# Optimization experiments

Measured on AMD Instinct MI355X. Metric: run time of the kernel, lower is better.

The kernel has to match this reference:

```python
import jax, jax.numpy as jnp
import numpy as np

N_NODES = 50000
N_EDGES = 600000
IN_DIM = 128
HID = 256
OUT = 3


def setup_inputs() -> dict:
    key = jax.random.key(0)
    ks = jax.random.split(key, 10)
    x = jax.random.normal(ks[0], (N_NODES, IN_DIM), dtype=jnp.float32)
    edge_index = jax.random.randint(ks[1], (2, N_EDGES), 0, N_NODES, dtype=jnp.int64)
    s = lambda k, shp: jax.random.normal(k, shp, dtype=jnp.float32) * (1.0 / np.sqrt(shp[0]))
    return {
        "x": x,
        "edge_index": edge_index,
        # SAGEConv1: lin_l (applied to aggregated neighbors, with bias), lin_r (root, no bias)
        "W1l": s(ks[2], (IN_DIM, HID)), "b1": jnp.zeros((HID,), jnp.float32), "W1r": s(ks[3], (IN_DIM, HID)),
        # SAGEConv2
        "W2l": s(ks[4], (HID, HID)), "b2": jnp.zeros((HID,), jnp.float32), "W2r": s(ks[5], (HID, HID)),
        # classification head
        "Wh": s(ks[6], (HID, OUT)), "bh": jnp.zeros((OUT,), jnp.float32),
    }


def _sage_conv(x, edge_index, Wl, b, Wr):
    """PyG SAGEConv with mean aggregation: out = lin_l(mean_{j->i} x_j) + lin_r(x_i)."""
    src, dst = edge_index[0], edge_index[1]
    n = x.shape[0]
    # gather source features and scatter-mean onto targets
    msg_sum = jax.ops.segment_sum(x[src], dst, num_segments=n)          # [N, d]
    deg = jax.ops.segment_sum(jnp.ones((src.shape[0],), x.dtype), dst, num_segments=n)
    mean = msg_sum / jnp.maximum(deg, 1.0)[:, None]                      # isolated nodes -> 0
    return mean @ Wl + b + x @ Wr


def reference(x, edge_index, W1l, b1, W1r, W2l, b2, W2r, Wh, bh):
    h = jax.nn.relu(_sage_conv(x, edge_index, W1l, b1, W1r))
    # dropout(p=0.2) is identity in eval mode
    h = jax.nn.relu(_sage_conv(h, edge_index, W2l, b2, W2r))
    return h @ Wh + bh
```

## Files before the change

### kernel.cpp

```cpp
#include <hip/hip_runtime.h>
#include <hip/hip_bf16.h>

#define N_NODES 50000
#define N_EDGES 600000
#define IN_DIM 128
#define HID 256
#define OUT_DIM 3

#define SCAN_B 256
#define SCAN_NB ((N_NODES + SCAN_B - 1) / SCAN_B)

typedef __bf16 bf16x8 __attribute__((ext_vector_type(8)));
typedef float f32x4 __attribute__((ext_vector_type(4)));

static __device__ __forceinline__ unsigned short f2b(float f) {
    union { float f; unsigned u; } u; u.f = f;
    unsigned r = u.u + 0x7fffu + ((u.u >> 16) & 1u);
    return (unsigned short)(r >> 16);
}
static __device__ __forceinline__ float b2f(unsigned short b) {
    union { unsigned u; float f; } u; u.u = ((unsigned)b) << 16;
    return u.f;
}


__global__ void count_deg_kernel(const int* __restrict__ dst, int* __restrict__ counts) {
    int e = blockIdx.x * blockDim.x + threadIdx.x;
    if (e < N_EDGES) atomicAdd(&counts[dst[e]], 1);
}

__global__ __launch_bounds__(256) void block_sum_kernel(const int* __restrict__ counts,
                                                        int* __restrict__ partial) {
    int node = blockIdx.x * SCAN_B + threadIdx.x;
    int v = (node < N_NODES) ? counts[node] : 0;
#pragma unroll
    for (int off = 32; off > 0; off >>= 1) v += __shfl_down(v, off);
    __shared__ int ws[4];
    if ((threadIdx.x & 63) == 0) ws[threadIdx.x >> 6] = v;
    __syncthreads();
    if (threadIdx.x == 0) partial[blockIdx.x] = ws[0] + ws[1] + ws[2] + ws[3];
}

__global__ __launch_bounds__(256) void scan_partial_kernel(int* __restrict__ partial) {
    __shared__ int s[SCAN_B];
    int t = threadIdx.x;
    int v = (t < SCAN_NB) ? partial[t] : 0;
    s[t] = v;
    __syncthreads();
    for (int off = 1; off < SCAN_B; off <<= 1) {
        int u = (t >= off) ? s[t - off] : 0;
        __syncthreads();
        s[t] += u;
        __syncthreads();
    }
    if (t < SCAN_NB) partial[t] = s[t] - v;
}

__global__ __launch_bounds__(256) void write_rowptr_kernel(const int* __restrict__ counts,
                                                           const int* __restrict__ partial,
                                                           int* __restrict__ row_ptr) {
    __shared__ int s[SCAN_B];
    int t = threadIdx.x;
    int node = blockIdx.x * SCAN_B + t;
    int v = (node < N_NODES) ? counts[node] : 0;
    s[t] = v;
    __syncthreads();
    for (int off = 1; off < SCAN_B; off <<= 1) {
        int u = (t >= off) ? s[t - off] : 0;
        __syncthreads();
        s[t] += u;
        __syncthreads();
    }
    if (node < N_NODES) row_ptr[node] = partial[blockIdx.x] + s[t] - v;
    if (node == 0) row_ptr[N_NODES] = N_EDGES;
}

__global__ void fill_csr_kernel(const int* __restrict__ src, const int* __restrict__ dst,
                                const int* __restrict__ row_ptr, int* __restrict__ cursor,
                                int* __restrict__ csr_src) {
    int e = blockIdx.x * blockDim.x + threadIdx.x;
    if (e < N_EDGES) {
        int d = dst[e];
        int pos = atomicAdd(&cursor[d], 1);
        csr_src[row_ptr[d] + pos] = src[e];
    }
}


__global__ void cast_f2b_kernel(const float* __restrict__ in, unsigned short* __restrict__ out, int n) {
    int i = blockIdx.x * blockDim.x + threadIdx.x;
    if (i * 4 < n) {
        float4 v = ((const float4*)in)[i];
        ushort4 o;
        o.x = f2b(v.x); o.y = f2b(v.y); o.z = f2b(v.z); o.w = f2b(v.w);
        ((ushort4*)out)[i] = o;
    }
}

__global__ void tcast4_kernel(const float* __restrict__ W1l, const float* __restrict__ W1r,
                              const float* __restrict__ W2l, const float* __restrict__ W2r,
                              unsigned short* __restrict__ W1lt, unsigned short* __restrict__ W1rt,
                              unsigned short* __restrict__ W2lt, unsigned short* __restrict__ W2rt) {
    int i = blockIdx.x * blockDim.x + threadIdx.x;
    const float* in; unsigned short* out; int K, base;
    if (i < 32768)        { in = W1l; out = W1lt; K = IN_DIM; base = 0; }
    else if (i < 65536)   { in = W1r; out = W1rt; K = IN_DIM; base = 32768; }
    else if (i < 131072)  { in = W2l; out = W2lt; K = HID;    base = 65536; }
    else if (i < 196608)  { in = W2r; out = W2rt; K = HID;    base = 131072; }
    else return;
    int j = i - base;
    int k = j >> 8;
    int n = j & 255;
    out[(size_t)n * K + k] = f2b(in[j]);
}


template <int D>
__global__ __launch_bounds__(256) void agg_mean_b_kernel(const unsigned short* __restrict__ feat,
                                                         const int* __restrict__ row_ptr,
                                                         const int* __restrict__ csr_src,
                                                         unsigned short* __restrict__ out) {
    int node = blockIdx.x * 4 + (threadIdx.x >> 6);
    if (node >= N_NODES) return;
    int lane = threadIdx.x & 63;
    constexpr int VPT = D / 64;
    float acc[VPT];
#pragma unroll
    for (int v = 0; v < VPT; v++) acc[v] = 0.f;
    int beg = row_ptr[node], end = row_ptr[node + 1];
    int i = beg;
    if constexpr (VPT == 2) {
        for (; i + 4 <= end; i += 4) {
            int s0 = csr_src[i], s1 = csr_src[i + 1], s2 = csr_src[i + 2], s3 = csr_src[i + 3];
            unsigned v0 = ((const unsigned*)(feat + (size_t)s0 * D))[lane];
            unsigned v1 = ((const unsigned*)(feat + (size_t)s1 * D))[lane];
            unsigned v2 = ((const unsigned*)(feat + (size_t)s2 * D))[lane];
            unsigned v3 = ((const unsigned*)(feat + (size_t)s3 * D))[lane];
            acc[0] += b2f((unsigned short)(v0 & 0xffff)) + b2f((unsigned short)(v1 & 0xffff))
                    + b2f((unsigned short)(v2 & 0xffff)) + b2f((unsigned short)(v3 & 0xffff));
            acc[1] += b2f((unsigned short)(v0 >> 16)) + b2f((unsigned short)(v1 >> 16))
                    + b2f((unsigned short)(v2 >> 16)) + b2f((unsigned short)(v3 >> 16));
        }
        for (; i < end; i++) {
            unsigned v = ((const unsigned*)(feat + (size_t)csr_src[i] * D))[lane];
            acc[0] += b2f((unsigned short)(v & 0xffff));
            acc[1] += b2f((unsigned short)(v >> 16));
        }
    } else {
        for (; i + 4 <= end; i += 4) {
            int s0 = csr_src[i], s1 = csr_src[i + 1], s2 = csr_src[i + 2], s3 = csr_src[i + 3];
            uint2 v0 = ((const uint2*)(feat + (size_t)s0 * D))[lane];
            uint2 v1 = ((const uint2*)(feat + (size_t)s1 * D))[lane];
            uint2 v2 = ((const uint2*)(feat + (size_t)s2 * D))[lane];
            uint2 v3 = ((const uint2*)(feat + (size_t)s3 * D))[lane];
            acc[0] += b2f((unsigned short)(v0.x & 0xffff)) + b2f((unsigned short)(v1.x & 0xffff))
                    + b2f((unsigned short)(v2.x & 0xffff)) + b2f((unsigned short)(v3.x & 0xffff));
            acc[1] += b2f((unsigned short)(v0.x >> 16)) + b2f((unsigned short)(v1.x >> 16))
                    + b2f((unsigned short)(v2.x >> 16)) + b2f((unsigned short)(v3.x >> 16));
            acc[2] += b2f((unsigned short)(v0.y & 0xffff)) + b2f((unsigned short)(v1.y & 0xffff))
                    + b2f((unsigned short)(v2.y & 0xffff)) + b2f((unsigned short)(v3.y & 0xffff));
            acc[3] += b2f((unsigned short)(v0.y >> 16)) + b2f((unsigned short)(v1.y >> 16))
                    + b2f((unsigned short)(v2.y >> 16)) + b2f((unsigned short)(v3.y >> 16));
        }
        for (; i < end; i++) {
            uint2 v = ((const uint2*)(feat + (size_t)csr_src[i] * D))[lane];
            acc[0] += b2f((unsigned short)(v.x & 0xffff));
            acc[1] += b2f((unsigned short)(v.x >> 16));
            acc[2] += b2f((unsigned short)(v.y & 0xffff));
            acc[3] += b2f((unsigned short)(v.y >> 16));
        }
    }
    float inv = (end > beg) ? 1.0f / (float)(end - beg) : 0.0f;
    unsigned short* o = out + (size_t)node * D;
    if constexpr (VPT == 2) {
        unsigned pk = (unsigned)f2b(acc[0] * inv) | ((unsigned)f2b(acc[1] * inv) << 16);
        ((unsigned*)o)[lane] = pk;
    } else {
        uint2 pk;
        pk.x = (unsigned)f2b(acc[0] * inv) | ((unsigned)f2b(acc[1] * inv) << 16);
        pk.y = (unsigned)f2b(acc[2] * inv) | ((unsigned)f2b(acc[3] * inv) << 16);
        ((uint2*)o)[lane] = pk;
    }
}


__global__ __launch_bounds__(256) void gemm_mfma_kernel(
    const unsigned short* __restrict__ A0, const unsigned short* __restrict__ W0t,
    const unsigned short* __restrict__ A1, const unsigned short* __restrict__ W1t,
    const float* __restrict__ bias, unsigned short* __restrict__ out,
    int M, int K) {
    __shared__ unsigned short As[128][40];
    __shared__ unsigned short Bs[128][40];

    const int t = threadIdx.x;
    const int w = t >> 6;
    const int l = t & 63;
    const int quad = l >> 4;
    const int lr = l & 15;
    const int m0 = blockIdx.x * 128;
    const int n0 = blockIdx.y * 128;

    f32x4 acc[2][8];
    const f32x4 zero = {0.f, 0.f, 0.f, 0.f};
#pragma unroll
    for (int mt = 0; mt < 2; mt++)
#pragma unroll
        for (int nt = 0; nt < 8; nt++) acc[mt][nt] = zero;

    float bias_r[8];
#pragma unroll
    for (int nt = 0; nt < 8; nt++) bias_r[nt] = bias[n0 + nt * 16 + lr];

    const int ldr = t >> 2;
    const int lkb = (t & 3) * 8;

    for (int phase = 0; phase < 2; ++phase) {
        const unsigned short* A = phase ? A1 : A0;
        const unsigned short* Wt = phase ? W1t : W0t;
        for (int k0 = 0; k0 < K; k0 += 32) {
            __syncthreads();
#pragma unroll
            for (int it = 0; it < 2; ++it) {
                int r = ldr + it * 64;
                int gm = m0 + r;
                uint4 av = make_uint4(0u, 0u, 0u, 0u);
                if (gm < M) av = *(const uint4*)(A + (size_t)gm * K + k0 + lkb);
                *(uint4*)&As[r][lkb] = av;
                uint4 bv = *(const uint4*)(Wt + (size_t)(n0 + r) * K + k0 + lkb);
                *(uint4*)&Bs[r][lkb] = bv;
            }
            __syncthreads();
            bf16x8 a[2], b[8];
#pragma unroll
            for (int mt = 0; mt < 2; mt++)
                a[mt] = *(const bf16x8*)&As[w * 32 + mt * 16 + lr][quad * 8];
#pragma unroll
            for (int nt = 0; nt < 8; nt++)
                b[nt] = *(const bf16x8*)&Bs[nt * 16 + lr][quad * 8];
#pragma unroll
            for (int mt = 0; mt < 2; mt++)
#pragma unroll
                for (int nt = 0; nt < 8; nt++)
                    acc[mt][nt] = __builtin_amdgcn_mfma_f32_16x16x32_bf16(a[mt], b[nt], acc[mt][nt], 0, 0, 0);
        }
    }

#pragma unroll
    for (int mt = 0; mt < 2; mt++)
#pragma unroll
        for (int r = 0; r < 4; r++) {
            int gm = m0 + w * 32 + mt * 16 + quad * 4 + r;
            if (gm >= M) continue;
            unsigned short* orow = out + (size_t)gm * HID;
#pragma unroll
            for (int nt = 0; nt < 8; nt++) {
                int gn = n0 + nt * 16 + lr;
                float v = acc[mt][nt][r] + bias_r[nt];
                v = fmaxf(v, 0.f);
                orow[gn] = f2b(v);
            }
        }
}


__global__ __launch_bounds__(256) void gemm_mfma_head_kernel(
    const unsigned short* __restrict__ A0, const unsigned short* __restrict__ W0t,
    const unsigned short* __restrict__ A1, const unsigned short* __restrict__ W1t,
    const float* __restrict__ bias, const float* __restrict__ Wh,
    float* __restrict__ out, int M, int K) {
    __shared__ unsigned short As[128][40];
    __shared__ unsigned short Bs[128][40];

    const int t = threadIdx.x;
    const int w = t >> 6;
    const int l = t & 63;
    const int quad = l >> 4;
    const int lr = l & 15;
    const int m0 = blockIdx.x * 128;
    const int n0 = blockIdx.y * 128;

    f32x4 acc[2][8];
    const f32x4 zero = {0.f, 0.f, 0.f, 0.f};
#pragma unroll
    for (int mt = 0; mt < 2; mt++)
#pragma unroll
        for (int nt = 0; nt < 8; nt++) acc[mt][nt] = zero;

    float bias_r[8];
    float wh_r[8][3];
#pragma unroll
    for (int nt = 0; nt < 8; nt++) {
        int gn = n0 + nt * 16 + lr;
        bias_r[nt] = bias[gn];
        wh_r[nt][0] = Wh[gn * 3 + 0];
        wh_r[nt][1] = Wh[gn * 3 + 1];
        wh_r[nt][2] = Wh[gn * 3 + 2];
    }

    const int ldr = t >> 2;
    const int lkb = (t & 3) * 8;

    for (int phase = 0; phase < 2; ++phase) {
        const unsigned short* A = phase ? A1 : A0;
        const unsigned short* Wt = phase ? W1t : W0t;
        for (int k0 = 0; k0 < K; k0 += 32) {
            __syncthreads();
#pragma unroll
            for (int it = 0; it < 2; ++it) {
                int r = ldr + it * 64;
                int gm = m0 + r;
                uint4 av = make_uint4(0u, 0u, 0u, 0u);
                if (gm < M) av = *(const uint4*)(A + (size_t)gm * K + k0 + lkb);
                *(uint4*)&As[r][lkb] = av;
                uint4 bv = *(const uint4*)(Wt + (size_t)(n0 + r) * K + k0 + lkb);
                *(uint4*)&Bs[r][lkb] = bv;
            }
            __syncthreads();
            bf16x8 a[2], b[8];
#pragma unroll
            for (int mt = 0; mt < 2; mt++)
                a[mt] = *(const bf16x8*)&As[w * 32 + mt * 16 + lr][quad * 8];
#pragma unroll
            for (int nt = 0; nt < 8; nt++)
                b[nt] = *(const bf16x8*)&Bs[nt * 16 + lr][quad * 8];
#pragma unroll
            for (int mt = 0; mt < 2; mt++)
#pragma unroll
                for (int nt = 0; nt < 8; nt++)
                    acc[mt][nt] = __builtin_amdgcn_mfma_f32_16x16x32_bf16(a[mt], b[nt], acc[mt][nt], 0, 0, 0);
        }
    }

#pragma unroll
    for (int mt = 0; mt < 2; mt++)
#pragma unroll
        for (int r = 0; r < 4; r++) {
            int gm = m0 + w * 32 + mt * 16 + quad * 4 + r;
            float p0 = 0.f, p1 = 0.f, p2 = 0.f;
#pragma unroll
            for (int nt = 0; nt < 8; nt++) {
                float v = fmaxf(acc[mt][nt][r] + bias_r[nt], 0.f);
                p0 += v * wh_r[nt][0];
                p1 += v * wh_r[nt][1];
                p2 += v * wh_r[nt][2];
            }
#pragma unroll
            for (int off = 1; off < 16; off <<= 1) {
                p0 += __shfl_xor(p0, off);
                p1 += __shfl_xor(p1, off);
                p2 += __shfl_xor(p2, off);
            }
            if (lr == 0 && gm < M) {
                atomicAdd(&out[(size_t)gm * 3 + 0], p0);
                atomicAdd(&out[(size_t)gm * 3 + 1], p1);
                atomicAdd(&out[(size_t)gm * 3 + 2], p2);
            }
        }
}

__global__ void init_out_kernel(const float* __restrict__ bh, float* __restrict__ out) {
    int i = blockIdx.x * blockDim.x + threadIdx.x;
    if (i < N_NODES * 3) {
        int c = i % 3;
        out[i] = bh[c];
    }
}


extern "C" void kernel_launch(void* const* d_in, const int* in_sizes, int n_in,
                              void* d_out, int out_size, void* d_ws, size_t ws_size,
                              hipStream_t stream) {
    const float* x   = (const float*)d_in[0];
    const int*   ei  = (const int*)d_in[1];
    const int*   src = ei;
    const int*   dst = ei + N_EDGES;
    const float* W1l = (const float*)d_in[2];
    const float* b1  = (const float*)d_in[3];
    const float* W1r = (const float*)d_in[4];
    const float* W2l = (const float*)d_in[5];
    const float* b2  = (const float*)d_in[6];
    const float* W2r = (const float*)d_in[7];
    const float* Wh  = (const float*)d_in[8];
    const float* bh  = (const float*)d_in[9];
    float* out = (float*)d_out;

    char* ws = (char*)d_ws;
    size_t off = 0;
    auto alloc = [&](size_t bytes) -> void* {
        void* p = ws + off;
        off = (off + bytes + 255) & ~(size_t)255;
        return p;
    };
    int* counts   = (int*)alloc((size_t)N_NODES * 4);
    int* row_ptr  = (int*)alloc((size_t)(N_NODES + 1) * 4);
    int* cursor   = (int*)alloc((size_t)N_NODES * 4);
    int* partial  = (int*)alloc((size_t)SCAN_NB * 4);
    int* csr_src  = (int*)alloc((size_t)N_EDGES * 4);
    unsigned short* xb   = (unsigned short*)alloc((size_t)N_NODES * IN_DIM * 2);
    unsigned short* agg  = (unsigned short*)alloc((size_t)N_NODES * HID * 2);
    unsigned short* h1   = (unsigned short*)alloc((size_t)N_NODES * HID * 2);
    unsigned short* W1lt = (unsigned short*)alloc((size_t)IN_DIM * HID * 2);
    unsigned short* W1rt = (unsigned short*)alloc((size_t)IN_DIM * HID * 2);
    unsigned short* W2lt = (unsigned short*)alloc((size_t)HID * HID * 2);
    unsigned short* W2rt = (unsigned short*)alloc((size_t)HID * HID * 2);

    hipMemsetAsync(counts, 0, (size_t)N_NODES * 4, stream);
    hipMemsetAsync(cursor, 0, (size_t)N_NODES * 4, stream);

    const int eblocks = (N_EDGES + 255) / 256;
    count_deg_kernel<<<eblocks, 256, 0, stream>>>(dst, counts);
    block_sum_kernel<<<SCAN_NB, SCAN_B, 0, stream>>>(counts, partial);
    scan_partial_kernel<<<1, SCAN_B, 0, stream>>>(partial);
    write_rowptr_kernel<<<SCAN_NB, SCAN_B, 0, stream>>>(counts, partial, row_ptr);
    fill_csr_kernel<<<eblocks, 256, 0, stream>>>(src, dst, row_ptr, cursor, csr_src);

    {
        int n = N_NODES * IN_DIM;
        cast_f2b_kernel<<<(n / 4 + 255) / 256, 256, 0, stream>>>(x, xb, n);
        tcast4_kernel<<<(196608 + 255) / 256, 256, 0, stream>>>(W1l, W1r, W2l, W2r,
                                                                W1lt, W1rt, W2lt, W2rt);
        init_out_kernel<<<(N_NODES * 3 + 255) / 256, 256, 0, stream>>>(bh, out);
    }

    const int nblocks4 = (N_NODES + 3) / 4;
    dim3 gg((N_NODES + 127) / 128, HID / 128);

    agg_mean_b_kernel<IN_DIM><<<nblocks4, 256, 0, stream>>>(xb, row_ptr, csr_src, agg);
    gemm_mfma_kernel<<<gg, 256, 0, stream>>>(agg, W1lt, xb, W1rt, b1, h1, N_NODES, IN_DIM);

    agg_mean_b_kernel<HID><<<nblocks4, 256, 0, stream>>>(h1, row_ptr, csr_src, agg);
    gemm_mfma_head_kernel<<<gg, 256, 0, stream>>>(agg, W2lt, h1, W2rt, b2, Wh, out, N_NODES, HID);
}
```

Baseline: 303.3 us.

## Use direct global-to-LDS loads in GEMM and 16-byte multi-edge gathers in aggregation

The GEMM kernels now stage tiles with global_load_lds (direct global-to-LDS DMA) into a k-block-major LDS layout, with a larger K step of 64 and two MFMA sub-steps per barrier pair. Activation buffers are padded to M_PAD rows so the row bounds check can be dropped. The aggregation kernels use 16-byte loads, with sub-groups of the wavefront handling different edges at once, then reduce across lanes with shuffles. This aims to cut per-load instruction overhead and barrier count. The risk is that the padded rows hold uninitialized data, which feeds only rows that are never stored.

Result: no change. 307.9 us (+1.5%).

```diff
diff --git a/kernel.cpp b/kernel.cpp
--- a/kernel.cpp
+++ b/kernel.cpp
@@ -7,6 +7,8 @@
 #define HID 256
 #define OUT_DIM 3
 
+#define M_PAD 50048
+
 #define SCAN_B 256
 #define SCAN_NB ((N_NODES + SCAN_B - 1) / SCAN_B)
 
@@ -21,6 +23,11 @@
 static __device__ __forceinline__ float b2f(unsigned short b) {
     union { unsigned u; float f; } u; u.u = ((unsigned)b) << 16;
     return u.f;
+}
+
+static __device__ __forceinline__ void gload16(const void* g, unsigned short* l) {
+    __builtin_amdgcn_global_load_lds((const __attribute__((address_space(1))) void*)g,
+                                     (__attribute__((address_space(3))) void*)l, 16, 0, 0);
 }
 
 
@@ -114,91 +121,156 @@
     out[(size_t)n * K + k] = f2b(in[j]);
 }
 
-
-template <int D>
-__global__ __launch_bounds__(256) void agg_mean_b_kernel(const unsigned short* __restrict__ feat,
-                                                         const int* __restrict__ row_ptr,
-                                                         const int* __restrict__ csr_src,
-                                                         unsigned short* __restrict__ out) {
+__global__ void init_out_kernel(const float* __restrict__ bh, float* __restrict__ out) {
+    int i = blockIdx.x * blockDim.x + threadIdx.x;
+    if (i < N_NODES * 3) out[i] = bh[i % 3];
+}
+
+
+static __device__ __forceinline__ void addv(float* acc, uint4 v) {
+    acc[0] += b2f((unsigned short)(v.x & 0xffff));
+    acc[1] += b2f((unsigned short)(v.x >> 16));
+    acc[2] += b2f((unsigned short)(v.y & 0xffff));
+    acc[3] += b2f((unsigned short)(v.y >> 16));
+    acc[4] += b2f((unsigned short)(v.z & 0xffff));
+    acc[5] += b2f((unsigned short)(v.z >> 16));
+    acc[6] += b2f((unsigned short)(v.w & 0xffff));
+    acc[7] += b2f((unsigned short)(v.w >> 16));
+}
+
+static __device__ __forceinline__ uint4 pack8(const float* a) {
+    uint4 pk;
+    pk.x = (unsigned)f2b(a[0]) | ((unsigned)f2b(a[1]) << 16);
+    pk.y = (unsigned)f2b(a[2]) | ((unsigned)f2b(a[3]) << 16);
+    pk.z = (unsigned)f2b(a[4]) | ((unsigned)f2b(a[5]) << 16);
+    pk.w = (unsigned)f2b(a[6]) | ((unsigned)f2b(a[7]) << 16);
+    return pk;
+}
+
+__global__ __launch_bounds__(256) void agg_mean256_kernel(const unsigned short* __restrict__ feat,
+                                                          const int* __restrict__ row_ptr,
+                                                          const int* __restrict__ csr_src,
+                                                          unsigned short* __restrict__ out) {
     int node = blockIdx.x * 4 + (threadIdx.x >> 6);
     if (node >= N_NODES) return;
     int lane = threadIdx.x & 63;
-    constexpr int VPT = D / 64;
-    float acc[VPT];
-#pragma unroll
-    for (int v = 0; v < VPT; v++) acc[v] = 0.f;
+    int half = lane >> 5, lh = lane & 31;
+    const uint4* f4 = (const uint4*)feat;
+    float acc[8];
+#pragma unroll
+    for (int j = 0; j < 8; j++) acc[j] = 0.f;
     int beg = row_ptr[node], end = row_ptr[node + 1];
     int i = beg;
-    if constexpr (VPT == 2) {
-        for (; i + 4 <= end; i += 4) {
-            int s0 = csr_src[i], s1 = csr_src[i + 1], s2 = csr_src[i + 2], s3 = csr_src[i + 3];
-            unsigned v0 = ((const unsigned*)(feat + (size_t)s0 * D))[lane];
-            unsigned v1 = ((const unsigned*)(feat + (size_t)s1 * D))[lane];
-            unsigned v2 = ((const unsigned*)(feat + (size_t)s2 * D))[lane];
-            unsigned v3 = ((const unsigned*)(feat + (size_t)s3 * D))[lane];
-            acc[0] += b2f((unsigned short)(v0 & 0xffff)) + b2f((unsigned short)(v1 & 0xffff))
-                    + b2f((unsigned short)(v2 & 0xffff)) + b2f((unsigned short)(v3 & 0xffff));
-            acc[1] += b2f((unsigned short)(v0 >> 16)) + b2f((unsigned short)(v1 >> 16))
-                    + b2f((unsigned short)(v2 >> 16)) + b2f((unsigned short)(v3 >> 16));
-        }
-        for (; i < end; i++) {
-            unsigned v = ((const unsigned*)(feat + (size_t)csr_src[i] * D))[lane];
-            acc[0] += b2f((unsigned short)(v & 0xffff));
-            acc[1] += b2f((unsigned short)(v >> 16));
-        }
-    } else {
-        for (; i + 4 <= end; i += 4) {
-            int s0 = csr_src[i], s1 = csr_src[i + 1], s2 = csr_src[i + 2], s3 = csr_src[i + 3];
-            uint2 v0 = ((const uint2*)(feat + (size_t)s0 * D))[lane];
-            uint2 v1 = ((const uint2*)(feat + (size_t)s1 * D))[lane];
-            uint2 v2 = ((const uint2*)(feat + (size_t)s2 * D))[lane];
-            uint2 v3 = ((const uint2*)(feat + (size_t)s3 * D))[lane];
-            acc[0] += b2f((unsigned short)(v0.x & 0xffff)) + b2f((unsigned short)(v1.x & 0xffff))
-                    + b2f((unsigned short)(v2.x & 0xffff)) + b2f((unsigned short)(v3.x & 0xffff));
-            acc[1] += b2f((unsigned short)(v0.x >> 16)) + b2f((unsigned short)(v1.x >> 16))
-                    + b2f((unsigned short)(v2.x >> 16)) + b2f((unsigned short)(v3.x >> 16));
-            acc[2] += b2f((unsigned short)(v0.y & 0xffff)) + b2f((unsigned short)(v1.y & 0xffff))
-                    + b2f((unsigned short)(v2.y & 0xffff)) + b2f((unsigned short)(v3.y & 0xffff));
-            acc[3] += b2f((unsigned short)(v0.y >> 16)) + b2f((unsigned short)(v1.y >> 16))
-                    + b2f((unsigned short)(v2.y >> 16)) + b2f((unsigned short)(v3.y >> 16));
-        }
-        for (; i < end; i++) {
-            uint2 v = ((const uint2*)(feat + (size_t)csr_src[i] * D))[lane];
-            acc[0] += b2f((unsigned short)(v.x & 0xffff));
-            acc[1] += b2f((unsigned short)(v.x >> 16));
-            acc[2] += b2f((unsigned short)(v.y & 0xffff));
-            acc[3] += b2f((unsigned short)(v.y >> 16));
-        }
+    for (; i + 4 <= end; i += 4) {
+        int sA = csr_src[i + half];
+        int sB = csr_src[i + 2 + half];
+        uint4 vA = f4[(size_t)sA * 32 + lh];
+        uint4 vB = f4[(size_t)sB * 32 + lh];
+        addv(acc, vA);
+        addv(acc, vB);
+    }
+    if (i + 2 <= end) {
+        int s = csr_src[i + half];
+        addv(acc, f4[(size_t)s * 32 + lh]);
+        i += 2;
+    }
+    if (i < end && half == 0) {
+        int s = csr_src[i];
+        addv(acc, f4[(size_t)s * 32 + lh]);
     }
     float inv = (end > beg) ? 1.0f / (float)(end - beg) : 0.0f;
-    unsigned short* o = out + (size_t)node * D;
-    if constexpr (VPT == 2) {
-        unsigned pk = (unsigned)f2b(acc[0] * inv) | ((unsigned)f2b(acc[1] * inv) << 16);
-        ((unsigned*)o)[lane] = pk;
-    } else {
-        uint2 pk;
-        pk.x = (unsigned)f2b(acc[0] * inv) | ((unsigned)f2b(acc[1] * inv) << 16);
-        pk.y = (unsigned)f2b(acc[2] * inv) | ((unsigned)f2b(acc[3] * inv) << 16);
-        ((uint2*)o)[lane] = pk;
-    }
-}
-
+#pragma unroll
+    for (int j = 0; j < 8; j++) {
+        acc[j] += __shfl_xor(acc[j], 32);
+        acc[j] *= inv;
+    }
+    if (half == 0) ((uint4*)(out + (size_t)node * 256))[lh] = pack8(acc);
+}
+
+__global__ __launch_bounds__(256) void agg_mean128_kernel(const unsigned short* __restrict__ feat,
+                                                          const int* __restrict__ row_ptr,
+                                                          const int* __restrict__ csr_src,
+                                                          unsigned short* __restrict__ out) {
+    int node = blockIdx.x * 4 + (threadIdx.x >> 6);
+    if (node >= N_NODES) return;
+    int lane = threadIdx.x & 63;
+    int q = lane >> 4, lq = lane & 15;
+    const uint4* f4 = (const uint4*)feat;
+    float acc[8];
+#pragma unroll
+    for (int j = 0; j < 8; j++) acc[j] = 0.f;
+    int beg = row_ptr[node], end = row_ptr[node + 1];
+    int i = beg;
+    for (; i + 8 <= end; i += 8) {
+        int sA = csr_src[i + q];
+        int sB = csr_src[i + 4 + q];
+        uint4 vA = f4[(size_t)sA * 16 + lq];
+        uint4 vB = f4[(size_t)sB * 16 + lq];
+        addv(acc, vA);
+        addv(acc, vB);
+    }
+    if (i + 4 <= end) {
+        int s = csr_src[i + q];
+        addv(acc, f4[(size_t)s * 16 + lq]);
+        i += 4;
+    }
+    int rem = end - i;
+    if (q < rem) {
+        int s = csr_src[i + q];
+        addv(acc, f4[(size_t)s * 16 + lq]);
+    }
+    float inv = (end > beg) ? 1.0f / (float)(end - beg) : 0.0f;
+#pragma unroll
+    for (int j = 0; j < 8; j++) {
+        acc[j] += __shfl_xor(acc[j], 32);
+        acc[j] += __shfl_xor(acc[j], 16);
+        acc[j] *= inv;
+    }
+    if (q == 0) ((uint4*)(out + (size_t)node * 128))[lq] = pack8(acc);
+}
+
+
+#define GEMM_STAGE_AND_MFMA(A, Wt)                                                          \
+    for (int k0 = 0; k0 < K; k0 += 64) {                                                    \
+        __syncthreads();                                                                    \
+        _Pragma("unroll")                                                                   \
+        for (int r = 0; r < 4; r++) {                                                       \
+            int kb = skb + 2 * r;                                                           \
+            gload16(A + (size_t)(m0 + sm) * K + k0 + kb * 8, &As[kb * 1024 + sm * 8]);      \
+            gload16(Wt + (size_t)(n0 + sm) * K + k0 + kb * 8, &Bs[kb * 1024 + sm * 8]);     \
+        }                                                                                   \
+        __syncthreads();                                                                    \
+        _Pragma("unroll")                                                                   \
+        for (int kk = 0; kk < 2; kk++) {                                                    \
+            int kbb = kk * 4 + quad;                                                        \
+            bf16x8 a[2], b[8];                                                              \
+            a[0] = *(const bf16x8*)&As[kbb * 1024 + (w * 32 + lr) * 8];                     \
+            a[1] = *(const bf16x8*)&As[kbb * 1024 + (w * 32 + 16 + lr) * 8];                \
+            _Pragma("unroll")                                                               \
+            for (int nt = 0; nt < 8; nt++)                                                  \
+                b[nt] = *(const bf16x8*)&Bs[kbb * 1024 + (nt * 16 + lr) * 8];               \
+            _Pragma("unroll")                                                               \
+            for (int mt = 0; mt < 2; mt++)                                                  \
+                _Pragma("unroll")                                                           \
+                for (int nt = 0; nt < 8; nt++)                                              \
+                    acc[mt][nt] = __builtin_amdgcn_mfma_f32_16x16x32_bf16(a[mt], b[nt],     \
+                                                                          acc[mt][nt], 0, 0, 0); \
+        }                                                                                   \
+    }
 
 __global__ __launch_bounds__(256) void gemm_mfma_kernel(
     const unsigned short* __restrict__ A0, const unsigned short* __restrict__ W0t,
     const unsigned short* __restrict__ A1, const unsigned short* __restrict__ W1t,
     const float* __restrict__ bias, unsigned short* __restrict__ out,
     int M, int K) {
-    __shared__ unsigned short As[128][40];
-    __shared__ unsigned short Bs[128][40];
+    __shared__ __align__(16) unsigned short As[8 * 128 * 8];
+    __shared__ __align__(16) unsigned short Bs[8 * 128 * 8];
 
     const int t = threadIdx.x;
-    const int w = t >> 6;
-    const int l = t & 63;
-    const int quad = l >> 4;
-    const int lr = l & 15;
-    const int m0 = blockIdx.x * 128;
-    const int n0 = blockIdx.y * 128;
+    const int w = t >> 6, l = t & 63;
+    const int quad = l >> 4, lr = l & 15;
+    const int m0 = blockIdx.x * 128, n0 = blockIdx.y * 128;
+    const int sm = t & 127, skb = t >> 7;
 
     f32x4 acc[2][8];
     const f32x4 zero = {0.f, 0.f, 0.f, 0.f};
@@ -211,39 +283,8 @@
 #pragma unroll
     for (int nt = 0; nt < 8; nt++) bias_r[nt] = bias[n0 + nt * 16 + lr];
 
-    const int ldr = t >> 2;
-    const int lkb = (t & 3) * 8;
-
-    for (int phase = 0; phase < 2; ++phase) {
-        const unsigned short* A = phase ? A1 : A0;
-        const unsigned short* Wt = phase ? W1t : W0t;
-        for (int k0 = 0; k0 < K; k0 += 32) {
-            __syncthreads();
-#pragma unroll
-            for (int it = 0; it < 2; ++it) {
-                int r = ldr + it * 64;
-                int gm = m0 + r;
-                uint4 av = make_uint4(0u, 0u, 0u, 0u);
-                if (gm < M) av = *(const uint4*)(A + (size_t)gm * K + k0 + lkb);
-                *(uint4*)&As[r][lkb] = av;
-                uint4 bv = *(const uint4*)(Wt + (size_t)(n0 + r) * K + k0 + lkb);
-                *(uint4*)&Bs[r][lkb] = bv;
-            }
-            __syncthreads();
-            bf16x8 a[2], b[8];
-#pragma unroll
-            for (int mt = 0; mt < 2; mt++)
-                a[mt] = *(const bf16x8*)&As[w * 32 + mt * 16 + lr][quad * 8];
-#pragma unroll
-            for (int nt = 0; nt < 8; nt++)
-                b[nt] = *(const bf16x8*)&Bs[nt * 16 + lr][quad * 8];
-#pragma unroll
-            for (int mt = 0; mt < 2; mt++)
-#pragma unroll
-                for (int nt = 0; nt < 8; nt++)
-                    acc[mt][nt] = __builtin_amdgcn_mfma_f32_16x16x32_bf16(a[mt], b[nt], acc[mt][nt], 0, 0, 0);
-        }
-    }
+    GEMM_STAGE_AND_MFMA(A0, W0t)
+    GEMM_STAGE_AND_MFMA(A1, W1t)
 
 #pragma unroll
     for (int mt = 0; mt < 2; mt++)
@@ -254,30 +295,25 @@
             unsigned short* orow = out + (size_t)gm * HID;
 #pragma unroll
             for (int nt = 0; nt < 8; nt++) {
-                int gn = n0 + nt * 16 + lr;
-                float v = acc[mt][nt][r] + bias_r[nt];
-                v = fmaxf(v, 0.f);
-                orow[gn] = f2b(v);
+                float v = fmaxf(acc[mt][nt][r] + bias_r[nt], 0.f);
+                orow[n0 + nt * 16 + lr] = f2b(v);
             }
         }
 }
-
 
 __global__ __launch_bounds__(256) void gemm_mfma_head_kernel(
     const unsigned short* __restrict__ A0, const unsigned short* __restrict__ W0t,
     const unsigned short* __restrict__ A1, const unsigned short* __restrict__ W1t,
     const float* __restrict__ bias, const float* __restrict__ Wh,
     float* __restrict__ out, int M, int K) {
-    __shared__ unsigned short As[128][40];
-    __shared__ unsigned short Bs[128][40];
+    __shared__ __align__(16) unsigned short As[8 * 128 * 8];
+    __shared__ __align__(16) unsigned short Bs[8 * 128 * 8];
 
     const int t = threadIdx.x;
-    const int w = t >> 6;
-    const int l = t & 63;
-    const int quad = l >> 4;
-    const int lr = l & 15;
-    const int m0 = blockIdx.x * 128;
-    const int n0 = blockIdx.y * 128;
+    const int w = t >> 6, l = t & 63;
+    const int quad = l >> 4, lr = l & 15;
+    const int m0 = blockIdx.x * 128, n0 = blockIdx.y * 128;
+    const int sm = t & 127, skb = t >> 7;
 
     f32x4 acc[2][8];
     const f32x4 zero = {0.f, 0.f, 0.f, 0.f};
@@ -297,39 +333,8 @@
         wh_r[nt][2] = Wh[gn * 3 + 2];
     }
 
-    const int ldr = t >> 2;
-    const int lkb = (t & 3) * 8;
-
-    for (int phase = 0; phase < 2; ++phase) {
-        const unsigned short* A = phase ? A1 : A0;
-        const unsigned short* Wt = phase ? W1t : W0t;
-        for (int k0 = 0; k0 < K; k0 += 32) {
-            __syncthreads();
-#pragma unroll
-            for (int it = 0; it < 2; ++it) {
-                int r = ldr + it * 64;
-                int gm = m0 + r;
-                uint4 av = make_uint4(0u, 0u, 0u, 0u);
-                if (gm < M) av = *(const uint4*)(A + (size_t)gm * K + k0 + lkb);
-                *(uint4*)&As[r][lkb] = av;
-                uint4 bv = *(const uint4*)(Wt + (size_t)(n0 + r) * K + k0 + lkb);
-                *(uint4*)&Bs[r][lkb] = bv;
-            }
-            __syncthreads();
-            bf16x8 a[2], b[8];
-#pragma unroll
-            for (int mt = 0; mt < 2; mt++)
-                a[mt] = *(const bf16x8*)&As[w * 32 + mt * 16 + lr][quad * 8];
-#pragma unroll
-            for (int nt = 0; nt < 8; nt++)
-                b[nt] = *(const bf16x8*)&Bs[nt * 16 + lr][quad * 8];
-#pragma unroll
-            for (int mt = 0; mt < 2; mt++)
-#pragma unroll
-                for (int nt = 0; nt < 8; nt++)
-                    acc[mt][nt] = __builtin_amdgcn_mfma_f32_16x16x32_bf16(a[mt], b[nt], acc[mt][nt], 0, 0, 0);
-        }
-    }
+    GEMM_STAGE_AND_MFMA(A0, W0t)
+    GEMM_STAGE_AND_MFMA(A1, W1t)
 
 #pragma unroll
     for (int mt = 0; mt < 2; mt++)
@@ -356,14 +361,6 @@
                 atomicAdd(&out[(size_t)gm * 3 + 2], p2);
             }
         }
-}
-
-__global__ void init_out_kernel(const float* __restrict__ bh, float* __restrict__ out) {
-    int i = blockIdx.x * blockDim.x + threadIdx.x;
-    if (i < N_NODES * 3) {
-        int c = i % 3;
-        out[i] = bh[c];
-    }
 }
 
 
@@ -396,9 +393,9 @@
     int* cursor   = (int*)alloc((size_t)N_NODES * 4);
     int* partial  = (int*)alloc((size_t)SCAN_NB * 4);
     int* csr_src  = (int*)alloc((size_t)N_EDGES * 4);
-    unsigned short* xb   = (unsigned short*)alloc((size_t)N_NODES * IN_DIM * 2);
-    unsigned short* agg  = (unsigned short*)alloc((size_t)N_NODES * HID * 2);
-    unsigned short* h1   = (unsigned short*)alloc((size_t)N_NODES * HID * 2);
+    unsigned short* xb   = (unsigned short*)alloc((size_t)M_PAD * IN_DIM * 2);
+    unsigned short* agg  = (unsigned short*)alloc((size_t)M_PAD * HID * 2);
+    unsigned short* h1   = (unsigned short*)alloc((size_t)M_PAD * HID * 2);
     unsigned short* W1lt = (unsigned short*)alloc((size_t)IN_DIM * HID * 2);
     unsigned short* W1rt = (unsigned short*)alloc((size_t)IN_DIM * HID * 2);
     unsigned short* W2lt = (unsigned short*)alloc((size_t)HID * HID * 2);
@@ -425,9 +422,9 @@
     const int nblocks4 = (N_NODES + 3) / 4;
     dim3 gg((N_NODES + 127) / 128, HID / 128);
 
-    agg_mean_b_kernel<IN_DIM><<<nblocks4, 256, 0, stream>>>(xb, row_ptr, csr_src, agg);
+    agg_mean128_kernel<<<nblocks4, 256, 0, stream>>>(xb, row_ptr, csr_src, agg);
     gemm_mfma_kernel<<<gg, 256, 0, stream>>>(agg, W1lt, xb, W1rt, b1, h1, N_NODES, IN_DIM);
 
-    agg_mean_b_kernel<HID><<<nblocks4, 256, 0, stream>>>(h1, row_ptr, csr_src, agg);
+    agg_mean256_kernel<<<nblocks4, 256, 0, stream>>>(h1, row_ptr, csr_src, agg);
     gemm_mfma_head_kernel<<<gg, 256, 0, stream>>>(agg, W2lt, h1, W2rt, b2, Wh, out, N_NODES, HID);
 }
```
